# Optimization experiments

Measured on AMD Instinct MI355X. Metric: run time of the kernel, lower is better.

## Reference

```python
import jax, jax.numpy as jnp
import numpy as np

DIM = 128
HEADS = 8
WIN = 4
B, D, H, W = 2, 48, 48, 48


def setup_inputs() -> dict:
    key = jax.random.key(0)
    k1, k2, k3 = jax.random.split(key, 3)
    x = jax.random.normal(k1, (B, DIM, D, H, W), dtype=jnp.float32)
    # torch.nn.Linear default init ~ U(-1/sqrt(fan_in), 1/sqrt(fan_in)); scaled normal is fine
    Wqkv = jax.random.normal(k2, (3 * DIM, DIM), dtype=jnp.float32) * (DIM ** -0.5)
    Wout = jax.random.normal(k3, (DIM, DIM), dtype=jnp.float32) * (DIM ** -0.5)
    bout = jnp.zeros((DIM,), dtype=jnp.float32)
    return {"x": x, "Wqkv": Wqkv, "Wout": Wout, "bout": bout}


def reference(x, Wqkv, Wout, bout):
    b, c, d, h, w = x.shape
    heads, win = HEADS, WIN
    hd = c // heads
    scale = c ** (-0.5)  # NOTE: original scales by dim**-0.5, not head_dim**-0.5
    nd, nh, nw = d // win, h // win, w // win

    xf = jnp.transpose(x, (0, 2, 3, 4, 1))          # (B,D,H,W,C)
    qkv = jnp.einsum('bdhwc,ec->bdhwe', xf, Wqkv)    # (B,D,H,W,3C)
    q, k, v = jnp.split(qkv, 3, axis=-1)

    def to_windows(t):
        # (B,D,H,W,C) -> (B,heads,num_windows,tokens,head_dim) matching unfold3d ordering
        t = t.reshape(b, nd, win, nh, win, nw, win, heads, hd)
        t = jnp.transpose(t, (0, 7, 1, 3, 5, 2, 4, 6, 8))  # B,hds,nd,nh,nw,wd,wh,ww,hd
        return t.reshape(b, heads, nd * nh * nw, win ** 3, hd)

    qw, kw, vw = to_windows(q), to_windows(k), to_windows(v)

    attn = jax.nn.softmax(jnp.einsum('bhntd,bhnsd->bhnts', qw, kw) * scale, axis=-1)
    out = jnp.einsum('bhnts,bhnsd->bhntd', attn, vw)  # (B,heads,N,T,hd)

    # Faithful to original: tokens stay in window order, then reinterpreted as spatial
    out = out.reshape(b, heads, -1, hd)
    out = jnp.transpose(out, (0, 2, 1, 3)).reshape(b, -1, heads * hd)
    out = out @ Wout.T + bout                         # (B, D*H*W, C)
    out = out.reshape(b, d, h, w, c)
    return jnp.transpose(out, (0, 4, 1, 2, 3))        # (B,C,D,H,W)
```

## Files before the change

### kernel.cpp

```cpp
#include <hip/hip_runtime.h>
#include <hip/hip_bf16.h>
#include <stdint.h>

#define NWIN 1728
#define SPD  110592

typedef __attribute__((ext_vector_type(8)))  short  short8;
typedef __attribute__((ext_vector_type(4)))  short  short4v;
typedef __attribute__((ext_vector_type(4)))  float  f32x4;
typedef __attribute__((ext_vector_type(16))) float  f32x16;

#define SRS 136
#define SQS 24
#define SVS 72

#define CFENCE() asm volatile("" ::: "memory")
#define LFENCE() asm volatile("s_waitcnt lgkmcnt(0)" ::: "memory")

__device__ __forceinline__ short f2bf(float f) {
  uint32_t u = __builtin_bit_cast(uint32_t, f);
  u += 0x7FFFu + ((u >> 16) & 1u);
  return (short)(u >> 16);
}

__global__ void cvt_weights_kernel(const float* __restrict__ wqkv,
                                   const float* __restrict__ wout,
                                   short* __restrict__ wq_bf,
                                   short* __restrict__ wo_bf) {
  int i = blockIdx.x * 256 + threadIdx.x;
  wq_bf[i] = f2bf(wqkv[i]);
  if (i < 128 * 128) wo_bf[i] = f2bf(wout[i]);
}

__global__ __launch_bounds__(256, 3)
void win_attn_kernel(const float* __restrict__ x,
                     const short* __restrict__ wqkv_bf,
                     const short* __restrict__ wout_bf,
                     const float* __restrict__ bout,
                     float* __restrict__ out) {
  __shared__ __align__(16) short sU[4 * 32 * SVS];
  __shared__ __align__(16) short sq[4][64 * SQS];
  __shared__ __align__(16) short sk[4][64 * SQS];
  __shared__ __align__(16) short sv[4][16 * SVS];

  const int tid  = threadIdx.x;
  const int lane = tid & 63;
  const int w    = tid >> 6;
  const int m16 = lane & 15, q16 = lane >> 4;
  const int m32 = lane & 31, h32 = lane >> 5;

  const int blk  = blockIdx.x;
  const int g    = (blk & 7) * 432 + (blk >> 3);
  const int b    = g / NWIN;
  const int win  = g - b * NWIN;
  const int id   = win / 144;
  const int ihw  = win - id * 144;
  const int ih   = ihw / 12;
  const int iw   = ihw - ih * 12;

  short* sR  = sU;
  short* spw = sU + w * (32 * SVS);

  short8 wcur[4];
  #pragma unroll
  for (int ks = 0; ks < 4; ++ks)
    wcur[ks] = *reinterpret_cast<const short8*>(
        wqkv_bf + ((2 * w) * 16 + m16) * 128 + ks * 32 + q16 * 8);

  const float* xb = x + (size_t)b * (128 * SPD) + id * (4 * 2304) + ih * (4 * 48) + iw * 4;
  float4 xv[4][2];
  #pragma unroll
  for (int i = 0; i < 4; ++i) {
    int row = i * 4 + w;
    const float* base = xb + (size_t)(lane * 2) * SPD + (row >> 2) * 2304 + (row & 3) * 48;
    xv[i][0] = *reinterpret_cast<const float4*>(base);
    xv[i][1] = *reinterpret_cast<const float4*>(base + SPD);
  }
  uint32_t* sRw = reinterpret_cast<uint32_t*>(sR);
  #pragma unroll
  for (int i = 0; i < 4; ++i) {
    int row = i * 4 + w;
    int cp  = lane;
    int t = (row >> 2) * 16 + (row & 3) * 4;
    const float4 v0 = xv[i][0], v1 = xv[i][1];
    sRw[(t + 0) * (SRS / 2) + cp] = (uint32_t)(uint16_t)f2bf(v0.x) | ((uint32_t)(uint16_t)f2bf(v1.x) << 16);
    sRw[(t + 1) * (SRS / 2) + cp] = (uint32_t)(uint16_t)f2bf(v0.y) | ((uint32_t)(uint16_t)f2bf(v1.y) << 16);
    sRw[(t + 2) * (SRS / 2) + cp] = (uint32_t)(uint16_t)f2bf(v0.z) | ((uint32_t)(uint16_t)f2bf(v1.z) << 16);
    sRw[(t + 3) * (SRS / 2) + cp] = (uint32_t)(uint16_t)f2bf(v0.w) | ((uint32_t)(uint16_t)f2bf(v1.w) << 16);
  }
  __syncthreads();

  short8 afrag[4][4];
  #pragma unroll
  for (int mt = 0; mt < 4; ++mt)
    #pragma unroll
    for (int ks = 0; ks < 4; ++ks)
      afrag[mt][ks] = *reinterpret_cast<const short8*>(
          &sR[(mt * 16 + m16) * SRS + ks * 32 + q16 * 8]);
  __syncthreads();

  f32x4 oacc[2][4];

  const float scale = 0.08838834764831845f;
  f32x16 z16;
  #pragma unroll
  for (int i = 0; i < 16; ++i) z16[i] = 0.0f;
  f32x4 z4;
  #pragma unroll
  for (int i = 0; i < 4; ++i) z4[i] = 0.0f;
  short8 ones8;
  #pragma unroll
  for (int i = 0; i < 8; ++i) ones8[i] = (short)0x3F80;

  #pragma unroll
  for (int hh = 0; hh < 2; ++hh) {
    const int h = 2 * w + hh;

    #pragma unroll
    for (int which = 0; which < 3; ++which) {
      short8 wnext[4];
      const bool have_next = !(hh == 1 && which == 2);
      if (have_next) {
        const int net = (which < 2) ? ((which + 1) * 8 + h)
                                    : (2 * w + 1);
        #pragma unroll
        for (int ks = 0; ks < 4; ++ks)
          wnext[ks] = *reinterpret_cast<const short8*>(
              wqkv_bf + (net * 16 + m16) * 128 + ks * 32 + q16 * 8);
      }
      f32x4 acc[4];
      #pragma unroll
      for (int mt = 0; mt < 4; ++mt)
        #pragma unroll
        for (int r = 0; r < 4; ++r) acc[mt][r] = 0.0f;
      #pragma unroll
      for (int ks = 0; ks < 4; ++ks)
        #pragma unroll
        for (int mt = 0; mt < 4; ++mt)
          acc[mt] = __builtin_amdgcn_mfma_f32_16x16x32_bf16(afrag[mt][ks], wcur[ks], acc[mt], 0, 0, 0);

      if (which == 0) {
        #pragma unroll
        for (int mt = 0; mt < 4; ++mt)
          #pragma unroll
          for (int r = 0; r < 4; ++r)
            sq[w][(mt * 16 + q16 * 4 + r) * SQS + m16] = f2bf(acc[mt][r]);
      } else if (which == 1) {
        #pragma unroll
        for (int mt = 0; mt < 4; ++mt)
          #pragma unroll
          for (int r = 0; r < 4; ++r)
            sk[w][(mt * 16 + q16 * 4 + r) * SQS + m16] = f2bf(acc[mt][r]);
      } else {
        #pragma unroll
        for (int mt = 0; mt < 4; ++mt) {
          short4v pk;
          pk[0] = f2bf(acc[mt][0]); pk[1] = f2bf(acc[mt][1]);
          pk[2] = f2bf(acc[mt][2]); pk[3] = f2bf(acc[mt][3]);
          *reinterpret_cast<short4v*>(&sv[w][m16 * SVS + mt * 16 + q16 * 4]) = pk;
        }
      }
      if (have_next) {
        #pragma unroll
        for (int ks = 0; ks < 4; ++ks) wcur[ks] = wnext[ks];
      }
    }
    LFENCE();

    short8 kf0 = *reinterpret_cast<const short8*>(&sk[w][(m32) * SQS + h32 * 8]);
    short8 kf1 = *reinterpret_cast<const short8*>(&sk[w][(32 + m32) * SQS + h32 * 8]);
    short8 vf0 = *reinterpret_cast<const short8*>(&sv[w][m16 * SVS + q16 * 8]);
    short8 vf1 = *reinterpret_cast<const short8*>(&sv[w][m16 * SVS + 32 + q16 * 8]);
    #pragma unroll
    for (int mt2 = 0; mt2 < 2; ++mt2) {
      short8 qf = *reinterpret_cast<const short8*>(&sq[w][(mt2 * 32 + m32) * SQS + h32 * 8]);
      f32x16 s0 = __builtin_amdgcn_mfma_f32_32x32x16_bf16(qf, kf0, z16, 0, 0, 0);
      f32x16 s1 = __builtin_amdgcn_mfma_f32_32x32x16_bf16(qf, kf1, z16, 0, 0, 0);
      CFENCE();
      #pragma unroll
      for (int r = 0; r < 16; ++r) {
        int row = (r & 3) + 8 * (r >> 2) + 4 * h32;
        spw[row * SVS + m32]      = f2bf(__expf(s0[r] * scale));
        spw[row * SVS + 32 + m32] = f2bf(__expf(s1[r] * scale));
      }
      LFENCE();
      #pragma unroll
      for (int sub = 0; sub < 2; ++sub) {
        short8 pf0 = *reinterpret_cast<const short8*>(&spw[(sub * 16 + m16) * SVS + q16 * 8]);
        short8 pf1 = *reinterpret_cast<const short8*>(&spw[(sub * 16 + m16) * SVS + 32 + q16 * 8]);
        int tile = mt2 * 2 + sub;
        f32x4 pv = __builtin_amdgcn_mfma_f32_16x16x32_bf16(pf0, vf0, z4, 0, 0, 0);
        pv       = __builtin_amdgcn_mfma_f32_16x16x32_bf16(pf1, vf1, pv, 0, 0, 0);
        f32x4 rs = __builtin_amdgcn_mfma_f32_16x16x32_bf16(pf0, ones8, z4, 0, 0, 0);
        rs       = __builtin_amdgcn_mfma_f32_16x16x32_bf16(pf1, ones8, rs, 0, 0, 0);
        #pragma unroll
        for (int r = 0; r < 4; ++r)
          oacc[hh][tile][r] = pv[r] * __builtin_amdgcn_rcpf(rs[r]);
      }
    }
  }

  short8 wob[2][4];
  #pragma unroll
  for (int ntl = 0; ntl < 2; ++ntl)
    #pragma unroll
    for (int ks = 0; ks < 4; ++ks)
      wob[ntl][ks] = *reinterpret_cast<const short8*>(
          wout_bf + ((2 * w + ntl) * 16 + m16) * 128 + ks * 32 + q16 * 8);
  float bias0 = bout[(2 * w) * 16 + m16];
  float bias1 = bout[(2 * w + 1) * 16 + m16];

  __syncthreads();

  #pragma unroll
  for (int hh = 0; hh < 2; ++hh) {
    int c0 = (2 * w + hh) * 16;
    #pragma unroll
    for (int mt = 0; mt < 4; ++mt)
      #pragma unroll
      for (int r = 0; r < 4; ++r)
        sR[(mt * 16 + q16 * 4 + r) * SRS + c0 + m16] = f2bf(oacc[hh][mt][r]);
  }
  __syncthreads();

  f32x4 outacc[4][2];
  #pragma unroll
  for (int i = 0; i < 4; ++i)
    #pragma unroll
    for (int j = 0; j < 2; ++j)
      #pragma unroll
      for (int r = 0; r < 4; ++r) outacc[i][j][r] = 0.0f;
  #pragma unroll
  for (int ks = 0; ks < 4; ++ks) {
    short8 af[4];
    #pragma unroll
    for (int mt = 0; mt < 4; ++mt)
      af[mt] = *reinterpret_cast<const short8*>(&sR[(mt * 16 + m16) * SRS + ks * 32 + q16 * 8]);
    #pragma unroll
    for (int ntl = 0; ntl < 2; ++ntl)
      #pragma unroll
      for (int mt = 0; mt < 4; ++mt)
        outacc[mt][ntl] = __builtin_amdgcn_mfma_f32_16x16x32_bf16(af[mt], wob[ntl][ks], outacc[mt][ntl], 0, 0, 0);
  }
  #pragma unroll
  for (int ntl = 0; ntl < 2; ++ntl) {
    int co = (2 * w + ntl) * 16 + m16;
    float bias = ntl ? bias1 : bias0;
    float* obase = out + (size_t)(b * 128 + co) * SPD + win * 64;
    #pragma unroll
    for (int mt = 0; mt < 4; ++mt) {
      float4 vres;
      vres.x = outacc[mt][ntl][0] + bias;
      vres.y = outacc[mt][ntl][1] + bias;
      vres.z = outacc[mt][ntl][2] + bias;
      vres.w = outacc[mt][ntl][3] + bias;
      *reinterpret_cast<float4*>(obase + mt * 16 + q16 * 4) = vres;
    }
  }
}

extern "C" void kernel_launch(void* const* d_in, const int* in_sizes, int n_in,
                              void* d_out, int out_size, void* d_ws, size_t ws_size,
                              hipStream_t stream) {
  const float* x    = (const float*)d_in[0];
  const float* wqkv = (const float*)d_in[1];
  const float* wout = (const float*)d_in[2];
  const float* bout = (const float*)d_in[3];
  short* wq_bf = (short*)d_ws;
  short* wo_bf = (short*)((char*)d_ws + 98304);
  cvt_weights_kernel<<<192, 256, 0, stream>>>(wqkv, wout, wq_bf, wo_bf);
  win_attn_kernel<<<2 * NWIN, 256, 0, stream>>>(x, wq_bf, wo_bf, bout, (float*)d_out);
}
```

Before: 272.3 us.

## Software-pipeline QKV projection of next head with attention of current head

Restructures the per-warp two-head loop so Q/K/V fragments for the first head are loaded into registers, then the second head's QKV projection is issued before running attention on the first head. This lets the MFMA projection work overlap the exp/softmax and LDS round trips of the first head's attention. It raises register pressure because six extra fragments stay live across the projection, which could lower occupancy or cause spills.

```diff
diff --git a/kernel.cpp b/kernel.cpp
--- a/kernel.cpp
+++ b/kernel.cpp
@@ -99,7 +99,8 @@
           &sR[(mt * 16 + m16) * SRS + ks * 32 + q16 * 8]);
   __syncthreads();
 
-  f32x4 oacc[2][4];
+  f32x4 oacc0[4];
+  f32x4 oacc1[4];
 
   const float scale = 0.08838834764831845f;
   f32x16 z16;
@@ -112,17 +113,14 @@
   #pragma unroll
   for (int i = 0; i < 8; ++i) ones8[i] = (short)0x3F80;
 
-  #pragma unroll
-  for (int hh = 0; hh < 2; ++hh) {
-    const int h = 2 * w + hh;
-
+  auto do_qkv = [&](int h, bool pre) {
     #pragma unroll
     for (int which = 0; which < 3; ++which) {
       short8 wnext[4];
-      const bool have_next = !(hh == 1 && which == 2);
+      const bool have_next = (which < 2) || pre;
       if (have_next) {
         const int net = (which < 2) ? ((which + 1) * 8 + h)
-                                    : (2 * w + 1);
+                                    : (h + 1);
         #pragma unroll
         for (int ks = 0; ks < 4; ++ks)
           wnext[ks] = *reinterpret_cast<const short8*>(
@@ -165,15 +163,13 @@
         for (int ks = 0; ks < 4; ++ks) wcur[ks] = wnext[ks];
       }
     }
-    LFENCE();
-
-    short8 kf0 = *reinterpret_cast<const short8*>(&sk[w][(m32) * SQS + h32 * 8]);
-    short8 kf1 = *reinterpret_cast<const short8*>(&sk[w][(32 + m32) * SQS + h32 * 8]);
-    short8 vf0 = *reinterpret_cast<const short8*>(&sv[w][m16 * SVS + q16 * 8]);
-    short8 vf1 = *reinterpret_cast<const short8*>(&sv[w][m16 * SVS + 32 + q16 * 8]);
+  };
+
+  auto do_attn = [&](f32x4* oa, short8 qfA, short8 qfB, short8 kf0, short8 kf1,
+                     short8 vf0, short8 vf1) {
     #pragma unroll
     for (int mt2 = 0; mt2 < 2; ++mt2) {
-      short8 qf = *reinterpret_cast<const short8*>(&sq[w][(mt2 * 32 + m32) * SQS + h32 * 8]);
+      short8 qf = mt2 ? qfB : qfA;
       f32x16 s0 = __builtin_amdgcn_mfma_f32_32x32x16_bf16(qf, kf0, z16, 0, 0, 0);
       f32x16 s1 = __builtin_amdgcn_mfma_f32_32x32x16_bf16(qf, kf1, z16, 0, 0, 0);
       CFENCE();
@@ -195,10 +191,34 @@
         rs       = __builtin_amdgcn_mfma_f32_16x16x32_bf16(pf1, ones8, rs, 0, 0, 0);
         #pragma unroll
         for (int r = 0; r < 4; ++r)
-          oacc[hh][tile][r] = pv[r] * __builtin_amdgcn_rcpf(rs[r]);
+          oa[tile][r] = pv[r] * __builtin_amdgcn_rcpf(rs[r]);
       }
     }
-  }
+  };
+
+  do_qkv(2 * w, true);
+  LFENCE();
+
+  short8 kf0 = *reinterpret_cast<const short8*>(&sk[w][(m32) * SQS + h32 * 8]);
+  short8 kf1 = *reinterpret_cast<const short8*>(&sk[w][(32 + m32) * SQS + h32 * 8]);
+  short8 vf0 = *reinterpret_cast<const short8*>(&sv[w][m16 * SVS + q16 * 8]);
+  short8 vf1 = *reinterpret_cast<const short8*>(&sv[w][m16 * SVS + 32 + q16 * 8]);
+  short8 qfA = *reinterpret_cast<const short8*>(&sq[w][(m32) * SQS + h32 * 8]);
+  short8 qfB = *reinterpret_cast<const short8*>(&sq[w][(32 + m32) * SQS + h32 * 8]);
+
+  do_qkv(2 * w + 1, false);
+
+  do_attn(oacc0, qfA, qfB, kf0, kf1, vf0, vf1);
+
+  LFENCE();
+
+  kf0 = *reinterpret_cast<const short8*>(&sk[w][(m32) * SQS + h32 * 8]);
+  kf1 = *reinterpret_cast<const short8*>(&sk[w][(32 + m32) * SQS + h32 * 8]);
+  vf0 = *reinterpret_cast<const short8*>(&sv[w][m16 * SVS + q16 * 8]);
+  vf1 = *reinterpret_cast<const short8*>(&sv[w][m16 * SVS + 32 + q16 * 8]);
+  qfA = *reinterpret_cast<const short8*>(&sq[w][(m32) * SQS + h32 * 8]);
+  qfB = *reinterpret_cast<const short8*>(&sq[w][(32 + m32) * SQS + h32 * 8]);
+  do_attn(oacc1, qfA, qfB, kf0, kf1, vf0, vf1);
 
   short8 wob[2][4];
   #pragma unroll
@@ -215,11 +235,12 @@
   #pragma unroll
   for (int hh = 0; hh < 2; ++hh) {
     int c0 = (2 * w + hh) * 16;
+    const f32x4* oa = hh ? oacc1 : oacc0;
     #pragma unroll
     for (int mt = 0; mt < 4; ++mt)
       #pragma unroll
       for (int r = 0; r < 4; ++r)
-        sR[(mt * 16 + q16 * 4 + r) * SRS + c0 + m16] = f2bf(oacc[hh][mt][r]);
+        sR[(mt * 16 + q16 * 4 + r) * SRS + c0 + m16] = f2bf(oa[mt][r]);
   }
   __syncthreads();
 
```

Measured after the change: 278.1 us. 1.02x slower.
